# Performance work log

Measured on AMD Instinct MI355X. Metric: run time of the kernel, lower is better.

The kernel has to match this reference:

```python
import jax, jax.numpy as jnp
import numpy as np

B, T, H = 32, 512, 1024   # batch, seq, hidden
L = 512                   # max_seq_length (must be <= 512 for rel_pos_bias)
E = 2048                  # hidden * expansion_factor
S = 128                   # shared qk dim
SQRT_S = float(np.sqrt(S))
EPS = 1e-5


def setup_inputs() -> dict:
    key = jax.random.key(0)
    ks = jax.random.split(key, 9)
    return {
        "x": jax.random.normal(ks[0], (B, T, H), jnp.float32),
        "ln_w": jnp.ones((H,), jnp.float32),
        "ln_b": jnp.zeros((H,), jnp.float32),
        "uv_w": jax.random.normal(ks[1], (2 * E + S, H), jnp.float32) * 0.02,  # torch Linear [out,in]
        "uv_b": jnp.zeros((2 * E + S,), jnp.float32),
        "gamma": jax.random.uniform(ks[2], (2, S), jnp.float32),
        "beta": jax.random.uniform(ks[3], (2, S), jnp.float32),
        "w": jax.random.uniform(ks[4], (2 * L - 1,), jnp.float32),  # Toeplitz rel-pos table
        "o_w": jax.random.normal(ks[5], (H, E), jnp.float32) * 0.02,
        "o_b": jnp.zeros((H,), jnp.float32),
    }


def _rope(x):
    # x: [B, T, 2, S]; positions run along the seq dim (dim=1), faithful to GAU.rope
    half = x.shape[-1] // 2
    pos = jnp.arange(x.shape[1], dtype=x.dtype)
    # note: original uses 10000**(+i/half) (increasing freq) — keep it faithful
    inv_freq = 10000.0 ** (jnp.arange(half, dtype=x.dtype) / half)
    sinusoid = pos[:, None] * inv_freq[None, :]          # [T, half]
    sin = jnp.sin(sinusoid)[None, :, None, :]            # [1, T, 1, half]
    cos = jnp.cos(sinusoid)[None, :, None, :]
    x1, x2 = jnp.split(x, 2, axis=-1)
    return jnp.concatenate([x1 * cos - x2 * sin, x2 * cos + x1 * sin], axis=-1)


def reference(x, ln_w, ln_b, uv_w, uv_b, gamma, beta, w, o_w, o_b):
    Tq = x.shape[1]
    shortcut = x  # hidden_size == output_size -> residual
    # LayerNorm
    mu = jnp.mean(x, axis=-1, keepdims=True)
    var = jnp.mean(jnp.square(x - mu), axis=-1, keepdims=True)
    xn = (x - mu) / jnp.sqrt(var + EPS) * ln_w + ln_b
    # fused uv projection + SiLU, then split into gate u, value v, base
    uv = jax.nn.silu(xn @ uv_w.T + uv_b)                  # [B, T, 2E+S]
    u, v, base = uv[..., :E], uv[..., E:2 * E], uv[..., 2 * E:]
    base = base[:, :, None, :] * gamma[None, None] + beta  # [B, T, 2, S]
    base = _rope(base)
    q, k = base[:, :, 0, :], base[:, :, 1, :]             # [B, T, S]
    qk = jnp.einsum('bis,bjs->bij', q, k)                 # [B, T, T]
    # Toeplitz rel-pos bias: bias[i, j] = w[j - i + L - 1]
    rel = jnp.arange(Tq)[None, :] - jnp.arange(Tq)[:, None] + (L - 1)
    bias = w[rel]                                         # [T, T]
    kernel = jnp.square(jax.nn.relu(qk / SQRT_S + bias[None]))  # squared-ReLU attention
    out = u * jnp.einsum('bij,bje->bie', kernel, v)       # gated attention output [B, T, E]
    return out @ o_w.T + o_b + shortcut
```

## Files before the change

### kernel.cpp

```cpp
#include <hip/hip_runtime.h>

typedef unsigned short u16;
typedef __bf16 bf16x8 __attribute__((ext_vector_type(8)));
typedef float f32x4 __attribute__((ext_vector_type(4)));

#define B_ 32
#define T_ 512
#define H_ 1024
#define E_ 2048
#define S_ 128

__device__ inline u16 f2bf(float f) {
  union { float f; unsigned int u; } c; c.f = f;
  unsigned int u = c.u;
  unsigned int r = (u + 0x7FFFu + ((u >> 16) & 1u)) >> 16;
  return (u16)r;
}
__device__ inline float bf2f(u16 h) {
  union { unsigned int u; float f; } c; c.u = ((unsigned int)h) << 16; return c.f;
}
__device__ inline float silu_fast(float v) {
  return v * __builtin_amdgcn_rcpf(1.0f + __expf(-v));
}

__device__ inline void g2lds16(const u16* g, u16* l) {
  __builtin_amdgcn_global_load_lds(
      (const __attribute__((address_space(1))) void*)g,
      (__attribute__((address_space(3))) void*)l, 16, 0, 0);
}

__global__ __launch_bounds__(256) void ln_kernel(const float* __restrict__ x,
                                                 const float* __restrict__ lw,
                                                 const float* __restrict__ lb,
                                                 u16* __restrict__ xn) {
  int row = blockIdx.x;
  int t = threadIdx.x;
  const float4* xr = (const float4*)(x + (size_t)row * H_);
  float4 v = xr[t];
  float s = v.x + v.y + v.z + v.w;
  float ss = v.x * v.x + v.y * v.y + v.z * v.z + v.w * v.w;
  for (int off = 1; off < 64; off <<= 1) {
    s += __shfl_xor(s, off);
    ss += __shfl_xor(ss, off);
  }
  __shared__ float red[8];
  int w = t >> 6, l = t & 63;
  if (l == 0) { red[w] = s; red[4 + w] = ss; }
  __syncthreads();
  s = red[0] + red[1] + red[2] + red[3];
  ss = red[4] + red[5] + red[6] + red[7];
  float mu = s * (1.0f / H_);
  float var = ss * (1.0f / H_) - mu * mu;
  float inv = rsqrtf(var + 1e-5f);
  int i = t * 4;
  ushort4 o;
  o.x = f2bf((v.x - mu) * inv * lw[i] + lb[i]);
  o.y = f2bf((v.y - mu) * inv * lw[i + 1] + lb[i + 1]);
  o.z = f2bf((v.z - mu) * inv * lw[i + 2] + lb[i + 2]);
  o.w = f2bf((v.w - mu) * inv * lw[i + 3] + lb[i + 3]);
  *(ushort4*)(xn + (size_t)row * H_ + i) = o;
}

__global__ void cvt_kernel(const float* __restrict__ in, u16* __restrict__ out, int n4) {
  int i = blockIdx.x * 256 + threadIdx.x;
  if (i < n4) {
    float4 v = ((const float4*)in)[i];
    ushort4 o;
    o.x = f2bf(v.x); o.y = f2bf(v.y); o.z = f2bf(v.z); o.w = f2bf(v.w);
    ((ushort4*)out)[i] = o;
  }
}

__global__ __launch_bounds__(256) void rope_kernel(const float* __restrict__ base,
                                                   const float* __restrict__ gamma,
                                                   const float* __restrict__ beta,
                                                   u16* __restrict__ q,
                                                   u16* __restrict__ k) {
  int row = blockIdx.x * 4 + (threadIdx.x >> 6);
  int s = threadIdx.x & 63;
  int t = row & (T_ - 1);
  const float* bp = base + (size_t)row * S_;
  float b1 = bp[s], b2 = bp[s + 64];
  float q1 = b1 * gamma[s] + beta[s];
  float q2 = b2 * gamma[64 + s] + beta[64 + s];
  float k1 = b1 * gamma[128 + s] + beta[128 + s];
  float k2 = b2 * gamma[192 + s] + beta[192 + s];
  float invf = (float)pow(10000.0, (double)s * (1.0 / 64.0));
  float ph = (float)t * invf;
  float sn, cs;
  sincosf(ph, &sn, &cs);
  size_t o = (size_t)row * S_;
  q[o + s]      = f2bf(q1 * cs - q2 * sn);
  q[o + 64 + s] = f2bf(q2 * cs + q1 * sn);
  k[o + s]      = f2bf(k1 * cs - k2 * sn);
  k[o + 64 + s] = f2bf(k2 * cs + k1 * sn);
}

template <int MODE>
__global__ __launch_bounds__(256)
void gemm_bt(const u16* __restrict__ A, const u16* __restrict__ Bm,
             int K, long long sA, long long sB,
             void* __restrict__ o0, void* __restrict__ o1, void* __restrict__ o2,
             const void* __restrict__ c0, const void* __restrict__ c1) {
  __shared__ __attribute__((aligned(16))) u16 lds[32768];
  u16* lsA = lds;
  u16* lsB = lds + 16384;

  const int z = blockIdx.z;
  const u16* Ab = A + (long long)z * sA;
  const u16* Bb = Bm + (long long)z * sB;
  const int m0 = blockIdx.y * 128;
  const int n0 = blockIdx.x * 128;
  const int t = threadIdx.x;
  const int w = t >> 6, l = t & 63;
  const int quad = l >> 4, l16 = l & 15;
  const int wm = (w >> 1) * 64, wn = (w & 1) * 64;
  const int srow = t >> 4;
  const int gl = (t & 15) ^ ((t >> 4) & 7);
  const int dst_off = t * 8;
  const int rsw = l16 & 7;

  f32x4 zero = {0.f, 0.f, 0.f, 0.f};
  f32x4 acc[4][4];
  for (int mi = 0; mi < 4; ++mi)
    for (int ni = 0; ni < 4; ++ni) acc[mi][ni] = zero;

  const u16* gA = Ab + ((size_t)(m0 + srow) * K + gl * 8);
  const u16* gB = Bb + ((size_t)(n0 + srow) * K + gl * 8);
  const size_t rK16 = (size_t)16 * K;

  for (int k0 = 0; k0 < K; k0 += 128) {
    __syncthreads();
#pragma unroll
    for (int c = 0; c < 8; ++c)
      g2lds16(gA + k0 + c * rK16, &lsA[c * 2048 + dst_off]);
#pragma unroll
    for (int c = 0; c < 8; ++c)
      g2lds16(gB + k0 + c * rK16, &lsB[c * 2048 + dst_off]);
    __syncthreads();
#pragma unroll
    for (int j = 0; j < 4; ++j) {
      int pg = ((j * 4 + quad) ^ rsw) * 8;
      bf16x8 af[4], bfr[4];
      for (int i = 0; i < 4; ++i) {
        af[i]  = *(const bf16x8*)&lsA[(wm + i * 16 + l16) * 128 + pg];
        bfr[i] = *(const bf16x8*)&lsB[(wn + i * 16 + l16) * 128 + pg];
      }
      for (int mi = 0; mi < 4; ++mi)
        for (int ni = 0; ni < 4; ++ni)
          acc[mi][ni] = __builtin_amdgcn_mfma_f32_16x16x32_bf16(af[mi], bfr[ni], acc[mi][ni], 0, 0, 0);
    }
  }

  if constexpr (MODE == 0) {
    const float* uvb = (const float*)c0;
    if (n0 < E_) {
      for (int mi = 0; mi < 4; ++mi)
        for (int ni = 0; ni < 4; ++ni) {
          int n = n0 + wn + ni * 16 + l16;
          float bias = uvb[n];
          for (int r = 0; r < 4; ++r) {
            int m = m0 + wm + mi * 16 + quad * 4 + r;
            ((u16*)o0)[(size_t)m * E_ + n] = f2bf(silu_fast(acc[mi][ni][r] + bias));
          }
        }
    } else if (n0 < 2 * E_) {
      const int bb = m0 >> 9;
      const int tt0 = m0 & (T_ - 1);
      const int nv0 = n0 - E_;
      for (int h = 0; h < 2; ++h) {
        __syncthreads();
        if ((w & 1) == h) {
          for (int mi = 0; mi < 4; ++mi)
            for (int ni = 0; ni < 4; ++ni) {
              int nl = ni * 16 + l16;
              float bias = uvb[n0 + h * 64 + nl];
              for (int r = 0; r < 4; ++r) {
                int ml = wm + mi * 16 + quad * 4 + r;
                u16 sv = f2bf(silu_fast(acc[mi][ni][r] + bias));
                int g = ml >> 3, o = ml & 7;
                int gs = g ^ (nl & 7);
                lds[nl * 128 + gs * 8 + o] = sv;
              }
            }
        }
        __syncthreads();
        int row = t >> 2;
        int q4 = t & 3;
        size_t gbase = ((size_t)bb * E_ + nv0 + h * 64 + row) * T_ + tt0;
        for (int gg = 0; gg < 4; ++gg) {
          int g = q4 * 4 + gg;
          int gsw = g ^ (row & 7);
          uint4 val = *(const uint4*)&lds[row * 128 + gsw * 8];
          *(uint4*)&(((u16*)o1)[gbase + g * 8]) = val;
        }
      }
    } else {
      for (int mi = 0; mi < 4; ++mi)
        for (int ni = 0; ni < 4; ++ni) {
          int n = n0 + wn + ni * 16 + l16;
          float bias = uvb[n];
          for (int r = 0; r < 4; ++r) {
            int m = m0 + wm + mi * 16 + quad * 4 + r;
            ((float*)o2)[(size_t)m * S_ + (n - 2 * E_)] = silu_fast(acc[mi][ni][r] + bias);
          }
        }
    }
  } else {
    for (int mi = 0; mi < 4; ++mi) {
      for (int ni = 0; ni < 4; ++ni) {
        int n = n0 + wn + ni * 16 + l16;
        for (int r = 0; r < 4; ++r) {
          int m = m0 + wm + mi * 16 + quad * 4 + r;
          float a = acc[mi][ni][r];
          if constexpr (MODE == 1) {
            const float* wrel = (const float*)c0;
            float v = a * 0.08838834764831845f + wrel[n - m + 511];
            v = fmaxf(v, 0.0f);
            ((u16*)o0)[(size_t)z * (T_ * T_) + (size_t)m * T_ + n] = f2bf(v * v);
          } else if constexpr (MODE == 2) {
            const u16* uu = (const u16*)c0;
            size_t gi = ((size_t)z * T_ + m) * E_ + n;
            float uv_ = bf2f(uu[gi]);
            ((u16*)o0)[gi] = f2bf(a * uv_);
          } else {
            const float* ob = (const float*)c0;
            const float* xs = (const float*)c1;
            size_t gi = (size_t)m * H_ + n;
            ((float*)o0)[gi] = a + ob[n] + xs[gi];
          }
        }
      }
    }
  }
}

extern "C" void kernel_launch(void* const* d_in, const int* in_sizes, int n_in,
                              void* d_out, int out_size, void* d_ws, size_t ws_size,
                              hipStream_t stream) {
  const float* x     = (const float*)d_in[0];
  const float* ln_w  = (const float*)d_in[1];
  const float* ln_b  = (const float*)d_in[2];
  const float* uv_w  = (const float*)d_in[3];
  const float* uv_b  = (const float*)d_in[4];
  const float* gamma = (const float*)d_in[5];
  const float* beta  = (const float*)d_in[6];
  const float* wrel  = (const float*)d_in[7];
  const float* o_w   = (const float*)d_in[8];
  const float* o_b   = (const float*)d_in[9];

  char* ws = (char*)d_ws;
  u16*   xn   = (u16*)(ws);
  u16*   qb   = (u16*)(ws);
  u16*   kb   = (u16*)(ws + 4194304);
  u16*   km   = (u16*)(ws + 8388608);
  u16*   uvwb = (u16*)(ws + 33554432);
  u16*   owb  = (u16*)(ws + 42205184);
  u16*   u    = (u16*)(ws + 46399488);
  u16*   vt   = (u16*)(ws + 113508352);
  float* base = (float*)(ws + 180617216);
  u16*   attn = u;

  ln_kernel<<<16384, 256, 0, stream>>>(x, ln_w, ln_b, xn);
  cvt_kernel<<<4224, 256, 0, stream>>>(uv_w, uvwb, 4224 * 1024 / 4);
  cvt_kernel<<<2048, 256, 0, stream>>>(o_w, owb, 1024 * 2048 / 4);
  gemm_bt<0><<<dim3(33, 128, 1), 256, 0, stream>>>(xn, uvwb, 1024, 0, 0,
                                                   u, vt, base, uv_b, nullptr);
  rope_kernel<<<4096, 256, 0, stream>>>(base, gamma, beta, qb, kb);
  gemm_bt<1><<<dim3(4, 4, 32), 256, 0, stream>>>(qb, kb, 128, 65536, 65536,
                                                 km, nullptr, nullptr, wrel, nullptr);
  gemm_bt<2><<<dim3(16, 4, 32), 256, 0, stream>>>(km, vt, 512, 262144, 1048576,
                                                  attn, nullptr, nullptr, u, nullptr);
  gemm_bt<3><<<dim3(8, 128, 1), 256, 0, stream>>>(attn, owb, 2048, 0, 0,
                                                  d_out, nullptr, nullptr, o_b, x);
}
```

Baseline: 541.1 us.

## Add 256x256-tile 512-thread GEMM with phased pipeline for big projections

Adds a new gemm256 kernel that computes 256x256 output tiles with 8 waves, double-buffered 128KB dynamic LDS, staged global-to-LDS prefetch two k-steps ahead, and barrier/setprio phases interleaving loads with MFMA groups. It also applies an optional XCD-aware block remap. It is used for the uv projection (with the base slice handled by the old kernel via a new column offset), the attention-times-V GEMM and the output projection. The goal is higher operand reuse per LDS load and better overlap of loads with MFMA, at the cost of more registers, fewer resident blocks and a fallback path if the large LDS allocation is refused.

After: 586.4 us. +8.4%, slower.

```diff
diff --git a/kernel.cpp b/kernel.cpp
--- a/kernel.cpp
+++ b/kernel.cpp
@@ -101,7 +101,7 @@
 void gemm_bt(const u16* __restrict__ A, const u16* __restrict__ Bm,
              int K, long long sA, long long sB,
              void* __restrict__ o0, void* __restrict__ o1, void* __restrict__ o2,
-             const void* __restrict__ c0, const void* __restrict__ c1) {
+             const void* __restrict__ c0, const void* __restrict__ c1, int nb0) {
   __shared__ __attribute__((aligned(16))) u16 lds[32768];
   u16* lsA = lds;
   u16* lsB = lds + 16384;
@@ -110,7 +110,7 @@
   const u16* Ab = A + (long long)z * sA;
   const u16* Bb = Bm + (long long)z * sB;
   const int m0 = blockIdx.y * 128;
-  const int n0 = blockIdx.x * 128;
+  const int n0 = nb0 + blockIdx.x * 128;
   const int t = threadIdx.x;
   const int w = t >> 6, l = t & 63;
   const int quad = l >> 4, l16 = l & 15;
@@ -235,6 +235,230 @@
   }
 }
 
+#define PH_SYNC()                                        \
+  __builtin_amdgcn_s_barrier();                          \
+  asm volatile("s_waitcnt lgkmcnt(0)" ::: "memory");     \
+  __builtin_amdgcn_sched_barrier(0);                     \
+  __builtin_amdgcn_s_setprio(1);
+
+#define PH_END()                                         \
+  __builtin_amdgcn_s_setprio(0);                         \
+  __builtin_amdgcn_s_barrier();
+
+#define MM2(mA, mB)                                                                                       \
+  _Pragma("unroll")                                                                                       \
+  for (int ni = 0; ni < 4; ++ni) {                                                                        \
+    acc[mA][ni] = __builtin_amdgcn_mfma_f32_16x16x32_bf16(af[mA][0], bfr[ni][0], acc[mA][ni], 0, 0, 0);   \
+    acc[mA][ni] = __builtin_amdgcn_mfma_f32_16x16x32_bf16(af[mA][1], bfr[ni][1], acc[mA][ni], 0, 0, 0);   \
+    acc[mB][ni] = __builtin_amdgcn_mfma_f32_16x16x32_bf16(af[mB][0], bfr[ni][0], acc[mB][ni], 0, 0, 0);   \
+    acc[mB][ni] = __builtin_amdgcn_mfma_f32_16x16x32_bf16(af[mB][1], bfr[ni][1], acc[mB][ni], 0, 0, 0);   \
+  }
+
+template <int MODE, bool XSWZ>
+__global__ __launch_bounds__(512, 2)
+void gemm256(const u16* __restrict__ A, const u16* __restrict__ Bm,
+             int K, long long sA, long long sB,
+             void* __restrict__ o0, void* __restrict__ o1,
+             const void* __restrict__ c0, const void* __restrict__ c1) {
+  extern __shared__ u16 lds[];
+
+  int bx = blockIdx.x, by = blockIdx.y;
+  if constexpr (XSWZ) {
+    int gx = gridDim.x;
+    int nwg = gx * gridDim.y;
+    int hh = by * gx + bx;
+    int cpx = nwg >> 3;
+    int lid = (hh & 7) * cpx + (hh >> 3);
+    bx = lid % gx; by = lid / gx;
+  }
+  const int z = blockIdx.z;
+  const u16* Ab = A + (long long)z * sA;
+  const u16* Bb = Bm + (long long)z * sB;
+  const int m0 = by * 256;
+  const int n0 = bx * 256;
+  const int t = threadIdx.x;
+  const int w = t >> 6, ln = t & 63;
+  const int quad = ln >> 4, l16 = ln & 15;
+  const int wm = w >> 2, wn = w & 3;
+
+  const int nkt = K >> 6;
+
+  const int goff = ((t & 7) ^ (((t >> 3) & 1) << 2)) * 8;
+  const u16* gA = Ab + (size_t)(m0 + (t >> 3)) * K + goff;
+  const u16* gB = Bb + (size_t)(n0 + (t >> 3)) * K + goff;
+  u16* ldst = lds + t * 8;
+  const size_t rK64 = (size_t)64 * K;
+  const size_t rK128 = (size_t)128 * K;
+
+  auto SA = [&](int b, int h, int kt) {
+    const u16* g = gA + h * rK128 + (size_t)kt * 64;
+    u16* d = ldst + b * 16384 + h * 8192;
+    g2lds16(g, d);
+    g2lds16(g + rK64, d + 4096);
+  };
+  auto SB = [&](int b, int h, int kt) {
+    const u16* g = gB + h * rK128 + (size_t)kt * 64;
+    u16* d = ldst + 32768 + b * 16384 + h * 8192;
+    g2lds16(g, d);
+    g2lds16(g + rK64, d + 4096);
+  };
+
+  f32x4 zero = {0.f, 0.f, 0.f, 0.f};
+  f32x4 acc[8][4];
+#pragma unroll
+  for (int mi = 0; mi < 8; ++mi)
+#pragma unroll
+    for (int ni = 0; ni < 4; ++ni) acc[mi][ni] = zero;
+
+  SA(0, 0, 0); SA(0, 1, 0); SB(0, 0, 0); SB(0, 1, 0);
+  if (nkt > 1) {
+    SB(1, 0, 1); SB(1, 1, 1); SA(1, 0, 1);
+    asm volatile("s_waitcnt vmcnt(6)" ::: "memory");
+  } else {
+    asm volatile("s_waitcnt vmcnt(0)" ::: "memory");
+  }
+  __builtin_amdgcn_s_barrier();
+
+  const u16* lA0 = lds + wm * 8192 + l16 * 64;
+  const u16* lB0 = lds + 32768 + (wn >> 1) * 8192 + ((wn & 1) * 64 + l16) * 64;
+  const int pg0 = (quad ^ ((l16 & 1) << 2)) * 8;
+  const int pg1 = ((4 + quad) ^ ((l16 & 1) << 2)) * 8;
+
+  bf16x8 bfr[4][2];
+  bf16x8 af[8][2];
+
+  for (int kt = 0; kt < nkt; ++kt) {
+    const int b = kt & 1;
+    const u16* lA = lA0 + b * 16384;
+    const u16* lB = lB0 + b * 16384;
+    const bool s2 = (kt + 2 < nkt);
+
+#pragma unroll
+    for (int ni = 0; ni < 4; ++ni) {
+      bfr[ni][0] = *(const bf16x8*)&lB[ni * 1024 + pg0];
+      bfr[ni][1] = *(const bf16x8*)&lB[ni * 1024 + pg1];
+    }
+#pragma unroll
+    for (int mi = 0; mi < 2; ++mi) {
+      af[mi][0] = *(const bf16x8*)&lA[mi * 1024 + pg0];
+      af[mi][1] = *(const bf16x8*)&lA[mi * 1024 + pg1];
+    }
+    if (kt + 1 < nkt) SA(b ^ 1, 1, kt + 1);
+    PH_SYNC();
+    MM2(0, 1);
+    PH_END();
+
+#pragma unroll
+    for (int mi = 2; mi < 6; ++mi) {
+      af[mi][0] = *(const bf16x8*)&lA[mi * 1024 + pg0];
+      af[mi][1] = *(const bf16x8*)&lA[mi * 1024 + pg1];
+    }
+    if (s2) SB(b, 0, kt + 2);
+    PH_SYNC();
+    MM2(2, 3);
+    PH_END();
+
+#pragma unroll
+    for (int mi = 6; mi < 8; ++mi) {
+      af[mi][0] = *(const bf16x8*)&lA[mi * 1024 + pg0];
+      af[mi][1] = *(const bf16x8*)&lA[mi * 1024 + pg1];
+    }
+    if (s2) SB(b, 1, kt + 2);
+    PH_SYNC();
+    MM2(4, 5);
+    PH_END();
+
+    if (s2) {
+      SA(b, 0, kt + 2);
+      asm volatile("s_waitcnt vmcnt(6)" ::: "memory");
+    } else {
+      asm volatile("s_waitcnt vmcnt(0)" ::: "memory");
+    }
+    __builtin_amdgcn_s_barrier();
+    __builtin_amdgcn_s_setprio(1);
+    MM2(6, 7);
+    PH_END();
+  }
+
+  if constexpr (MODE == 0) {
+    const float* uvb = (const float*)c0;
+    if (n0 < E_) {
+#pragma unroll
+      for (int ni = 0; ni < 4; ++ni) {
+        int n = n0 + wn * 64 + ni * 16 + l16;
+        float bias = uvb[n];
+#pragma unroll
+        for (int mi = 0; mi < 8; ++mi)
+#pragma unroll
+          for (int r = 0; r < 4; ++r) {
+            int m = m0 + wm * 128 + mi * 16 + quad * 4 + r;
+            ((u16*)o0)[(size_t)m * E_ + n] = f2bf(silu_fast(acc[mi][ni][r] + bias));
+          }
+      }
+    } else {
+      const int bb = m0 >> 9;
+      const int tt0 = m0 & (T_ - 1);
+      const int nv0 = n0 - E_;
+#pragma unroll
+      for (int ni = 0; ni < 4; ++ni) {
+        int nl = wn * 64 + ni * 16 + l16;
+        float bias = uvb[n0 + nl];
+#pragma unroll
+        for (int mi = 0; mi < 8; ++mi)
+#pragma unroll
+          for (int r = 0; r < 4; ++r) {
+            int ml = wm * 128 + mi * 16 + quad * 4 + r;
+            u16 sv = f2bf(silu_fast(acc[mi][ni][r] + bias));
+            int g = ml >> 3, o = ml & 7;
+            lds[nl * 256 + ((g ^ (nl & 7)) << 3) + o] = sv;
+          }
+      }
+      __syncthreads();
+      int row = t >> 1;
+      u16* o1p = (u16*)o1;
+      size_t gbase = ((size_t)bb * E_ + nv0 + row) * T_ + tt0;
+#pragma unroll
+      for (int cc = 0; cc < 16; ++cc) {
+        int c = (t & 1) * 16 + cc;
+        int gs = c ^ (row & 7);
+        uint4 val = *(const uint4*)&lds[row * 256 + gs * 8];
+        *(uint4*)&o1p[gbase + c * 8] = val;
+      }
+    }
+  } else if constexpr (MODE == 2) {
+    const u16* uu = (const u16*)c0;
+#pragma unroll
+    for (int mi = 0; mi < 8; ++mi)
+#pragma unroll
+      for (int ni = 0; ni < 4; ++ni) {
+        int n = n0 + wn * 64 + ni * 16 + l16;
+#pragma unroll
+        for (int r = 0; r < 4; ++r) {
+          int m = m0 + wm * 128 + mi * 16 + quad * 4 + r;
+          size_t gi = ((size_t)z * T_ + m) * E_ + n;
+          float uv_ = bf2f(uu[gi]);
+          ((u16*)o0)[gi] = f2bf(acc[mi][ni][r] * uv_);
+        }
+      }
+  } else {
+    const float* ob = (const float*)c0;
+    const float* xs = (const float*)c1;
+#pragma unroll
+    for (int ni = 0; ni < 4; ++ni) {
+      int n = n0 + wn * 64 + ni * 16 + l16;
+      float bias = ob[n];
+#pragma unroll
+      for (int mi = 0; mi < 8; ++mi)
+#pragma unroll
+        for (int r = 0; r < 4; ++r) {
+          int m = m0 + wm * 128 + mi * 16 + quad * 4 + r;
+          size_t gi = (size_t)m * H_ + n;
+          ((float*)o0)[gi] = acc[mi][ni][r] + bias + xs[gi];
+        }
+    }
+  }
+}
+
 extern "C" void kernel_launch(void* const* d_in, const int* in_sizes, int n_in,
                               void* d_out, int out_size, void* d_ws, size_t ws_size,
                               hipStream_t stream) {
@@ -261,16 +485,42 @@
   float* base = (float*)(ws + 180617216);
   u16*   attn = u;
 
+  static int use256 = -1;
+  if (use256 < 0) {
+    auto* k0 = gemm256<0, true>;
+    auto* k2 = gemm256<2, false>;
+    auto* k3 = gemm256<3, true>;
+    hipError_t e0 = hipFuncSetAttribute((const void*)k0, hipFuncAttributeMaxDynamicSharedMemorySize, 131072);
+    hipError_t e2 = hipFuncSetAttribute((const void*)k2, hipFuncAttributeMaxDynamicSharedMemorySize, 131072);
+    hipError_t e3 = hipFuncSetAttribute((const void*)k3, hipFuncAttributeMaxDynamicSharedMemorySize, 131072);
+    use256 = (e0 == hipSuccess && e2 == hipSuccess && e3 == hipSuccess) ? 1 : 0;
+  }
+
   ln_kernel<<<16384, 256, 0, stream>>>(x, ln_w, ln_b, xn);
   cvt_kernel<<<4224, 256, 0, stream>>>(uv_w, uvwb, 4224 * 1024 / 4);
   cvt_kernel<<<2048, 256, 0, stream>>>(o_w, owb, 1024 * 2048 / 4);
-  gemm_bt<0><<<dim3(33, 128, 1), 256, 0, stream>>>(xn, uvwb, 1024, 0, 0,
-                                                   u, vt, base, uv_b, nullptr);
-  rope_kernel<<<4096, 256, 0, stream>>>(base, gamma, beta, qb, kb);
-  gemm_bt<1><<<dim3(4, 4, 32), 256, 0, stream>>>(qb, kb, 128, 65536, 65536,
-                                                 km, nullptr, nullptr, wrel, nullptr);
-  gemm_bt<2><<<dim3(16, 4, 32), 256, 0, stream>>>(km, vt, 512, 262144, 1048576,
-                                                  attn, nullptr, nullptr, u, nullptr);
-  gemm_bt<3><<<dim3(8, 128, 1), 256, 0, stream>>>(attn, owb, 2048, 0, 0,
-                                                  d_out, nullptr, nullptr, o_b, x);
-}
+
+  if (use256) {
+    gemm256<0, true><<<dim3(16, 64, 1), 512, 131072, stream>>>(
+        xn, uvwb, 1024, 0, 0, u, vt, uv_b, nullptr);
+    gemm_bt<0><<<dim3(1, 128, 1), 256, 0, stream>>>(
+        xn, uvwb, 1024, 0, 0, u, vt, base, uv_b, nullptr, 4096);
+    rope_kernel<<<4096, 256, 0, stream>>>(base, gamma, beta, qb, kb);
+    gemm_bt<1><<<dim3(4, 4, 32), 256, 0, stream>>>(
+        qb, kb, 128, 65536, 65536, km, nullptr, nullptr, wrel, nullptr, 0);
+    gemm256<2, false><<<dim3(8, 2, 32), 512, 131072, stream>>>(
+        km, vt, 512, 262144, 1048576, attn, nullptr, u, nullptr);
+    gemm256<3, true><<<dim3(4, 64, 1), 512, 131072, stream>>>(
+        attn, owb, 2048, 0, 0, d_out, nullptr, o_b, x);
+  } else {
+    gemm_bt<0><<<dim3(33, 128, 1), 256, 0, stream>>>(
+        xn, uvwb, 1024, 0, 0, u, vt, base, uv_b, nullptr, 0);
+    rope_kernel<<<4096, 256, 0, stream>>>(base, gamma, beta, qb, kb);
+    gemm_bt<1><<<dim3(4, 4, 32), 256, 0, stream>>>(
+        qb, kb, 128, 65536, 65536, km, nullptr, nullptr, wrel, nullptr, 0);
+    gemm_bt<2><<<dim3(16, 4, 32), 256, 0, stream>>>(
+        km, vt, 512, 262144, 1048576, attn, nullptr, nullptr, u, nullptr, 0);
+    gemm_bt<3><<<dim3(8, 128, 1), 256, 0, stream>>>(
+        attn, owb, 2048, 0, 0, d_out, nullptr, nullptr, o_b, x, 0);
+  }
+}
```
